# Performance work log

Measured on AMD Instinct MI355X. Metric: run time of the kernel, lower is better.

Reference implementation:

```python
import jax, jax.numpy as jnp
import numpy as np

B, LQ, LKV = 2, 2048, 2048
C, CTX, H, DK = 1024, 768, 16, 64
SCALE = DK ** (-0.5)


def setup_inputs() -> dict:
    key = jax.random.key(0)
    kx, ky, kq, kkv, kp, kb = jax.random.split(key, 6)
    # weights stored as [in, out] so projection is x @ W
    return {
        "x": jax.random.normal(kx, (B, LQ, C), dtype=jnp.float32),
        "y": jax.random.normal(ky, (B, LKV, CTX), dtype=jnp.float32),
        "Wq": jax.random.normal(kq, (C, H * DK), dtype=jnp.float32) * (C ** -0.5),
        "Wkv": jax.random.normal(kkv, (CTX, 2 * H * DK), dtype=jnp.float32) * (CTX ** -0.5),
        "Wproj": jax.random.normal(kp, (H * DK, C), dtype=jnp.float32) * ((H * DK) ** -0.5),
        "bproj": jax.random.normal(kb, (C,), dtype=jnp.float32) * 0.01,
    }


def reference(x, y, Wq, Wkv, Wproj, bproj):
    b, lq, _ = x.shape
    lkv = y.shape[1]
    # Q projection: [b, lq, H*DK] -> [b, H, lq, DK]
    q = (x @ Wq).reshape(b, lq, H, DK).transpose(0, 2, 1, 3)
    kv = (y @ Wkv).reshape(b, lkv, 2, H, DK).transpose(2, 0, 3, 1, 4)
    k, v = kv[0], kv[1]
    # attention scores [b, H, lq, lkv], stable softmax, no dropout (Identity)
    atten = jax.nn.softmax(jnp.einsum("bhid,bhjd->bhij", q, k) * SCALE, axis=-1)
    res = jnp.einsum("bhij,bhjd->bhid", atten, v)  # [b, H, lq, DK]
    res = res.transpose(0, 2, 1, 3).reshape(b, lq, H * DK)
    out = res @ Wproj + bproj  # [b, lq, C]
    return out
```

## Files before the change

kernel.cpp:

```cpp
#include <hip/hip_runtime.h>
#include <hip/hip_bf16.h>
#include <cstdint>

typedef unsigned short u16;
typedef __attribute__((ext_vector_type(4))) float f32x4;
typedef __attribute__((ext_vector_type(8))) short s16x8;
typedef __attribute__((ext_vector_type(4))) unsigned int u32x4;

#define B_    2
#define LQ_   2048
#define LKV_  2048
#define H_    16
#define QSCALE_ 0.18033688011112042f

__device__ __forceinline__ u16 f2b(float f) {
  union { float f; unsigned int u; } v; v.f = f;
  unsigned int r = v.u + 0x7fffu + ((v.u >> 16) & 1u);
  return (u16)(r >> 16);
}

__device__ __forceinline__ unsigned cvtpk(float lo, float hi) {
  unsigned r;
  asm("v_cvt_pk_bf16_f32 %0, %1, %2" : "=v"(r) : "v"(lo), "v"(hi));
  return r;
}

#if __has_builtin(__builtin_amdgcn_exp2f)
__device__ __forceinline__ float fexp2(float x) { return __builtin_amdgcn_exp2f(x); }
#else
__device__ __forceinline__ float fexp2(float x) {
  float r; asm volatile("v_exp_f32 %0, %1" : "=v"(r) : "v"(x)); return r;
}
#endif

#define GLOAD(g, l) __builtin_amdgcn_global_load_lds( \
    (const __attribute__((address_space(1))) void*)(g), \
    (__attribute__((address_space(3))) void*)(l), 16, 0, 0)

__global__ void prep(const float* __restrict__ x, u16* __restrict__ xb,
                     const float* __restrict__ y, u16* __restrict__ yb,
                     const float* __restrict__ Wq, u16* __restrict__ WqT,
                     const float* __restrict__ Wkv, u16* __restrict__ WkvT,
                     const float* __restrict__ Wp, u16* __restrict__ WpT) {
  __shared__ u16 tile[64][65];
  const int bid = blockIdx.x;
  const int t = threadIdx.x;
  if (bid < 7168) {
    const float* in; u16* out; int i;
    if (bid < 4096) { in = x; out = xb; i = (bid * 256 + t) * 4; }
    else            { in = y; out = yb; i = ((bid - 4096) * 256 + t) * 4; }
    float4 v = *reinterpret_cast<const float4*>(in + i);
    ushort4 r;
    r.x = f2b(v.x); r.y = f2b(v.y); r.z = f2b(v.z); r.w = f2b(v.w);
    *reinterpret_cast<ushort4*>(out + i) = r;
    return;
  }
  const int tb = bid - 7168;
  const float* W; u16* WT; int K, N, bx, by;
  if (tb < 256)      { W = Wq;  WT = WqT;  K = 1024; N = 1024; bx = tb & 15;         by = tb >> 4; }
  else if (tb < 640) { W = Wkv; WT = WkvT; K = 768;  N = 2048; bx = (tb - 256) & 31; by = (tb - 256) >> 5; }
  else               { W = Wp;  WT = WpT;  K = 1024; N = 1024; bx = (tb - 640) & 15; by = (tb - 640) >> 4; }
  const int n0 = bx * 64, k0 = by * 64;
#pragma unroll
  for (int p = 0; p < 4; ++p) {
    int r = (t >> 4) + p * 16;
    int c = (t & 15) * 4;
    float4 v = *reinterpret_cast<const float4*>(W + (size_t)(k0 + r) * N + n0 + c);
    tile[r][c + 0] = f2b(v.x);
    tile[r][c + 1] = f2b(v.y);
    tile[r][c + 2] = f2b(v.z);
    tile[r][c + 3] = f2b(v.w);
  }
  __syncthreads();
#pragma unroll
  for (int p = 0; p < 4; ++p) {
    int nr = (t >> 4) + p * 16;
    int kc = (t & 15) * 4;
    ushort4 o;
    o.x = tile[kc + 0][nr];
    o.y = tile[kc + 1][nr];
    o.z = tile[kc + 2][nr];
    o.w = tile[kc + 3][nr];
    *reinterpret_cast<ushort4*>(WT + (size_t)(n0 + nr) * K + k0 + kc) = o;
  }
}

template <int OM>
__global__ __launch_bounds__(256, 3)
void gemm_bt(const u16* __restrict__ A, const u16* __restrict__ BT,
             u16* __restrict__ Cb, float* __restrict__ Cf,
             const float* __restrict__ bias, u16* __restrict__ VTp,
             int M, int N, int K) {
  __shared__ __attribute__((aligned(16))) char smem[49152];
  const int tid = threadIdx.x;
  const int w = tid >> 6, lane = tid & 63;
  const int l16 = lane & 15, lk = lane >> 4;
  const int m0 = blockIdx.x * 128, n0 = blockIdx.y * 64;
  const int wm = w >> 1, ks = w & 1;
  const int K2 = K >> 1;
  const int NS = K2 >> 5;

  f32x4 acc[4][4];
#pragma unroll
  for (int i = 0; i < 4; ++i)
#pragma unroll
    for (int j = 0; j < 4; ++j)
      acc[i][j] = (f32x4){0.f, 0.f, 0.f, 0.f};

  const int srow = tid >> 2;
  const int sc = ((tid & 3) ^ ((tid >> 3) & 3)) * 8;
  const u16* gA0 = A + (size_t)(m0 + srow) * K + sc;
  const u16* gA1 = gA0 + K2;
  const u16* gB0 = BT + (size_t)(n0 + srow) * K + sc;
  const u16* gB1 = gB0 + K2;
  const size_t rstep = (size_t)64 * K;
  char* ldsA = smem;
  char* ldsB = smem + 32768;

  auto stage = [&](int k0, int bb) {
    GLOAD(gA0 + k0,         ldsA + bb * 8192 + w * 1024);
    GLOAD(gA0 + k0 + rstep, ldsA + bb * 8192 + 4096 + w * 1024);
    GLOAD(gA1 + k0,         ldsA + 16384 + bb * 8192 + w * 1024);
    GLOAD(gA1 + k0 + rstep, ldsA + 16384 + bb * 8192 + 4096 + w * 1024);
    GLOAD(gB0 + k0,         ldsB + bb * 4096 + w * 1024);
    GLOAD(gB1 + k0,         ldsB + 8192 + bb * 4096 + w * 1024);
  };

  const char* sAb = smem + ks * 16384;
  const char* sBb = smem + 32768 + ks * 8192;
  const int swl = ((l16 >> 1) & 3) << 4;

  stage(0, 0);
  __syncthreads();
  int cur = 0;
  for (int s = 0; s < NS; ++s) {
    if (s + 1 < NS) stage((s + 1) * 32, cur ^ 1);
    s16x8 af[4], bf[4];
#pragma unroll
    for (int mt = 0; mt < 4; ++mt)
      af[mt] = *reinterpret_cast<const s16x8*>(
          sAb + cur * 8192 + (wm * 64 + mt * 16 + l16) * 64 + ((lk * 16) ^ swl));
#pragma unroll
    for (int nt = 0; nt < 4; ++nt)
      bf[nt] = *reinterpret_cast<const s16x8*>(
          sBb + cur * 4096 + (nt * 16 + l16) * 64 + ((lk * 16) ^ swl));
    __builtin_amdgcn_s_setprio(1);
#pragma unroll
    for (int mt = 0; mt < 4; ++mt)
#pragma unroll
      for (int nt = 0; nt < 4; ++nt)
        acc[mt][nt] = __builtin_amdgcn_mfma_f32_16x16x32_bf16(af[mt], bf[nt], acc[mt][nt], 0, 0, 0);
    __builtin_amdgcn_s_setprio(0);
    __syncthreads();
    cur ^= 1;
  }

  if (ks == 1) {
    float* mb = reinterpret_cast<float*>(smem) + wm * 4096;
#pragma unroll
    for (int mt = 0; mt < 4; ++mt)
#pragma unroll
      for (int nt = 0; nt < 4; ++nt)
        *reinterpret_cast<f32x4*>(mb + ((mt * 4 + nt) * 64 + lane) * 4) = acc[mt][nt];
  }
  __syncthreads();
  if (ks == 1) return;
  {
    const float* mb = reinterpret_cast<const float*>(smem) + wm * 4096;
#pragma unroll
    for (int mt = 0; mt < 4; ++mt)
#pragma unroll
      for (int nt = 0; nt < 4; ++nt)
        acc[mt][nt] += *reinterpret_cast<const f32x4*>(mb + ((mt * 4 + nt) * 64 + lane) * 4);
  }

#pragma unroll
  for (int mt = 0; mt < 4; ++mt) {
#pragma unroll
    for (int nt = 0; nt < 4; ++nt) {
      const int col = n0 + nt * 16 + l16;
      const int row0 = m0 + wm * 64 + mt * 16 + lk * 4;
      if (OM == 2 && col >= 1024) {
        int b = row0 >> 11, kv = row0 & 2047;
        int h = (col >> 6) & 15, d = col & 63;
        ushort4 o;
        o.x = f2b(acc[mt][nt][0]); o.y = f2b(acc[mt][nt][1]);
        o.z = f2b(acc[mt][nt][2]); o.w = f2b(acc[mt][nt][3]);
        *reinterpret_cast<ushort4*>(VTp + (((size_t)(b * 16 + h) * 64 + d) * 2048 + kv)) = o;
      } else {
#pragma unroll
        for (int j = 0; j < 4; ++j) {
          int row = row0 + j;
          if (OM == 3)      Cb[(size_t)row * N + col] = f2b(acc[mt][nt][j] * QSCALE_);
          else if (OM == 2) Cb[(size_t)row * 1024 + col] = f2b(acc[mt][nt][j]);
          else              Cf[(size_t)row * N + col] = acc[mt][nt][j] + bias[col];
        }
      }
    }
  }
}

__global__ __launch_bounds__(512, 4)
void flash_attn(const u16* __restrict__ Kq, const u16* __restrict__ Qb,
                const u16* __restrict__ VT, u16* __restrict__ Rb) {
  __shared__ __attribute__((aligned(16))) char smem[65536];
  __shared__ float dmerge[512 * 2];

  const int tid = threadIdx.x;
  const int w = tid >> 6, l = tid & 63;
  const int l16 = l & 15, lk = l >> 4;
  const int half = w >> 2, w4 = w & 3;

  const int bid = blockIdx.x;
  const int wg = ((bid & 7) << 6) | (bid >> 3);
  const int qt = wg & 15, bh = wg >> 4;
  const int b = bh >> 4, h = bh & 15;
  const int qrow0 = qt * 128 + w4 * 32;

  const u16* qp = Qb + ((size_t)(b * LQ_ + qrow0 + l16)) * 1024 + h * 64;
  s16x8 qf[2][2];
#pragma unroll
  for (int g = 0; g < 2; ++g)
#pragma unroll
    for (int ksq = 0; ksq < 2; ++ksq)
      qf[g][ksq] = *reinterpret_cast<const s16x8*>(qp + g * 16 * 1024 + ksq * 32 + lk * 8);

  f32x4 Oacc[2][4], Osum[2];
#pragma unroll
  for (int g = 0; g < 2; ++g) {
    Osum[g] = (f32x4){0.f, 0.f, 0.f, 0.f};
#pragma unroll
    for (int dt = 0; dt < 4; ++dt) Oacc[g][dt] = (f32x4){0.f, 0.f, 0.f, 0.f};
  }

  const u16* Kg = Kq + ((size_t)(b * LKV_ + half * 1024)) * 1024 + h * 64;
  const u16* Vg = VT + ((size_t)bh * 64) * 2048 + half * 1024;
  char* Kl = smem + half * 32768;
  char* Vl = smem + half * 32768 + 16384;

  s16x8 ones;
#pragma unroll
  for (int i = 0; i < 8; ++i) ones[i] = (short)0x3F80;

  const int r0 = ((l16 >> 2) << 3) + (l16 & 3);
  const int swk = ((l16 & 3) | (((l16 >> 2) & 1) << 2)) << 4;
  const int swv = (l16 & 7) << 4;

  const int srow = (tid & 255) >> 3;
  const int sck = (tid & 7) ^ ((srow & 3) | (((srow >> 3) & 1) << 2));
  const int scv = (tid & 7) ^ (srow & 7);
  const u16* kp0 = Kg + (size_t)srow * 1024 + sck * 8;
  const u16* kp1 = kp0 + (size_t)32 * 1024;
  const u16* vp0 = Vg + (size_t)srow * 2048 + scv * 8;
  const u16* vp1 = vp0 + (size_t)32 * 2048;
  char* kd0 = Kl + w4 * 1024;
  char* vd0 = Vl + w4 * 1024;

  auto stage = [&](int bb) {
    GLOAD(kp0, kd0 + bb * 8192);
    GLOAD(kp1, kd0 + bb * 8192 + 4096);
    GLOAD(vp0, vd0 + bb * 8192);
    GLOAD(vp1, vd0 + bb * 8192 + 4096);
  };

  stage(0);
  kp0 += 65536; kp1 += 65536; vp0 += 64; vp1 += 64;
  __syncthreads();

  int cur = 0;
  for (int jt = 0; jt < 16; ++jt) {
    if (jt < 15) {
      stage(cur ^ 1);
      kp0 += 65536; kp1 += 65536; vp0 += 64; vp1 += 64;
    }
    const char* kb = Kl + cur * 8192;
    const char* vb = Vl + cur * 8192;

    f32x4 sacc[2][4];
#pragma unroll
    for (int g = 0; g < 2; ++g)
#pragma unroll
      for (int ct = 0; ct < 4; ++ct) sacc[g][ct] = (f32x4){0.f, 0.f, 0.f, 0.f};

    __builtin_amdgcn_s_setprio(1);
#pragma unroll
    for (int ct = 0; ct < 4; ++ct) {
      const int R = r0 + ((ct & 1) << 2) + ((ct >> 1) << 5);
      const char* rp = kb + R * 128;
      s16x8 ka0 = *reinterpret_cast<const s16x8*>(rp + ((lk * 16) ^ swk));
      s16x8 ka1 = *reinterpret_cast<const s16x8*>(rp + ((64 + lk * 16) ^ swk));
      sacc[0][ct] = __builtin_amdgcn_mfma_f32_16x16x32_bf16(ka0, qf[0][0], sacc[0][ct], 0, 0, 0);
      sacc[0][ct] = __builtin_amdgcn_mfma_f32_16x16x32_bf16(ka1, qf[0][1], sacc[0][ct], 0, 0, 0);
      sacc[1][ct] = __builtin_amdgcn_mfma_f32_16x16x32_bf16(ka0, qf[1][0], sacc[1][ct], 0, 0, 0);
      sacc[1][ct] = __builtin_amdgcn_mfma_f32_16x16x32_bf16(ka1, qf[1][1], sacc[1][ct], 0, 0, 0);
    }
    __builtin_amdgcn_s_setprio(0);

#pragma unroll
    for (int g = 0; g < 2; ++g)
#pragma unroll
      for (int ct = 0; ct < 4; ++ct)
#pragma unroll
        for (int j = 0; j < 4; ++j)
          sacc[g][ct][j] = fexp2(sacc[g][ct][j]);

#pragma unroll
    for (int f = 0; f < 2; ++f) {
      s16x8 va[4];
#pragma unroll
      for (int dt = 0; dt < 4; ++dt)
        va[dt] = *reinterpret_cast<const s16x8*>(vb + (dt * 16 + l16) * 128 + ((f * 64 + lk * 16) ^ swv));
      s16x8 pf[2];
#pragma unroll
      for (int g = 0; g < 2; ++g) {
        const f32x4 pA = sacc[g][2 * f];
        const f32x4 pB = sacc[g][2 * f + 1];
        union { unsigned u[4]; s16x8 v; } pk;
        pk.u[0] = cvtpk(pA[0], pA[1]);
        pk.u[1] = cvtpk(pA[2], pA[3]);
        pk.u[2] = cvtpk(pB[0], pB[1]);
        pk.u[3] = cvtpk(pB[2], pB[3]);
        pf[g] = pk.v;
      }
      __builtin_amdgcn_s_setprio(1);
#pragma unroll
      for (int dt = 0; dt < 4; ++dt) {
        Oacc[0][dt] = __builtin_amdgcn_mfma_f32_16x16x32_bf16(va[dt], pf[0], Oacc[0][dt], 0, 0, 0);
        Oacc[1][dt] = __builtin_amdgcn_mfma_f32_16x16x32_bf16(va[dt], pf[1], Oacc[1][dt], 0, 0, 0);
      }
      Osum[0] = __builtin_amdgcn_mfma_f32_16x16x32_bf16(ones, pf[0], Osum[0], 0, 0, 0);
      Osum[1] = __builtin_amdgcn_mfma_f32_16x16x32_bf16(ones, pf[1], Osum[1], 0, 0, 0);
      __builtin_amdgcn_s_setprio(0);
    }
    __syncthreads();
    cur ^= 1;
  }

  if (w >= 4) {
    char* mb = smem + (((w - 4) * 64 + l) * 128);
#pragma unroll
    for (int g = 0; g < 2; ++g)
#pragma unroll
      for (int dt = 0; dt < 4; ++dt)
        *reinterpret_cast<f32x4*>(mb + (((g * 4 + dt) * 16) ^ ((l & 7) << 4))) = Oacc[g][dt];
    dmerge[((w - 4) * 64 + l) * 2 + 0] = Osum[0][0];
    dmerge[((w - 4) * 64 + l) * 2 + 1] = Osum[1][0];
  }
  __syncthreads();
  if (w < 4) {
    const char* mb = smem + ((w * 64 + l) * 128);
#pragma unroll
    for (int g = 0; g < 2; ++g) {
      float inv = 1.f / (Osum[g][0] + dmerge[(w * 64 + l) * 2 + g]);
      u16* op = Rb + ((size_t)(b * LQ_ + qrow0 + g * 16 + l16)) * 1024 + h * 64 + lk * 4;
#pragma unroll
      for (int dt = 0; dt < 4; ++dt) {
        f32x4 o2 = *reinterpret_cast<const f32x4*>(mb + (((g * 4 + dt) * 16) ^ ((l & 7) << 4)));
        f32x4 s = Oacc[g][dt] + o2;
        ushort4 o;
        o.x = f2b(s[0] * inv); o.y = f2b(s[1] * inv);
        o.z = f2b(s[2] * inv); o.w = f2b(s[3] * inv);
        *reinterpret_cast<ushort4*>(op + dt * 16) = o;
      }
    }
  }
}

extern "C" void kernel_launch(void* const* d_in, const int* in_sizes, int n_in,
                              void* d_out, int out_size, void* d_ws, size_t ws_size,
                              hipStream_t stream) {
  const float* x   = (const float*)d_in[0];
  const float* y   = (const float*)d_in[1];
  const float* Wq  = (const float*)d_in[2];
  const float* Wkv = (const float*)d_in[3];
  const float* Wp  = (const float*)d_in[4];
  const float* bp  = (const float*)d_in[5];
  float* out = (float*)d_out;

  u16* p = (u16*)d_ws;
  u16* xb   = p; p += (size_t)4096 * 1024;
  u16* yb   = p; p += (size_t)4096 * 768;
  u16* WqT  = p; p += (size_t)1024 * 1024;
  u16* WkvT = p; p += (size_t)2048 * 768;
  u16* WpT  = p; p += (size_t)1024 * 1024;
  u16* Qb   = p; p += (size_t)4096 * 1024;
  u16* Kbf  = p; p += (size_t)4096 * 1024;
  u16* VTb  = p; p += (size_t)4096 * 1024;
  u16* Rb   = p; p += (size_t)4096 * 1024;

  prep<<<8064, 256, 0, stream>>>(x, xb, y, yb, Wq, WqT, Wkv, WkvT, Wp, WpT);

  gemm_bt<3><<<dim3(32, 16), 256, 0, stream>>>(xb, WqT, Qb, nullptr, nullptr, nullptr, 4096, 1024, 1024);
  gemm_bt<2><<<dim3(32, 32), 256, 0, stream>>>(yb, WkvT, Kbf, nullptr, nullptr, VTb, 4096, 2048, 768);
  flash_attn<<<512, 512, 0, stream>>>(Kbf, Qb, VTb, Rb);
  gemm_bt<1><<<dim3(32, 16), 256, 0, stream>>>(Rb, WpT, nullptr, out, bp, nullptr, 4096, 1024, 1024);
}
```

Baseline: 121.0 us.

## Merge Q and KV projection GEMMs into one launch and drop split-K warps

The Q and KV projection GEMMs now run as a single 1536-block launch, with the block index choosing which problem each block computes. This removes one kernel launch and its tail, and lets the two GEMMs fill the GPU together. The GEMM core also drops the intra-block split-K scheme (two K-halves plus an LDS reduction). Each of the 4 warps now owns a 64x32 output tile and works on a 64-wide K stage with a new 8-way XOR swizzle. This removes the reduction's LDS round trip and barrier, but gives each warp fewer MFMAs per fragment load.

```diff
diff --git a/kernel.cpp b/kernel.cpp
--- a/kernel.cpp
+++ b/kernel.cpp
@@ -85,100 +85,77 @@
   }
 }
 
-template <int OM>
-__global__ __launch_bounds__(256, 3)
-void gemm_bt(const u16* __restrict__ A, const u16* __restrict__ BT,
-             u16* __restrict__ Cb, float* __restrict__ Cf,
-             const float* __restrict__ bias, u16* __restrict__ VTp,
-             int M, int N, int K) {
-  __shared__ __attribute__((aligned(16))) char smem[49152];
+__device__ __forceinline__ void gemm_core(
+    int OM, const u16* __restrict__ A, const u16* __restrict__ BT,
+    u16* __restrict__ Cb, float* __restrict__ Cf,
+    const float* __restrict__ bias, u16* __restrict__ VTp,
+    int N, int K, int m0, int n0, char* smem) {
   const int tid = threadIdx.x;
   const int w = tid >> 6, lane = tid & 63;
   const int l16 = lane & 15, lk = lane >> 4;
-  const int m0 = blockIdx.x * 128, n0 = blockIdx.y * 64;
-  const int wm = w >> 1, ks = w & 1;
-  const int K2 = K >> 1;
-  const int NS = K2 >> 5;
-
-  f32x4 acc[4][4];
+  const int wm = w >> 1, wn = w & 1;
+  const int NS = K >> 6;
+
+  f32x4 acc[4][2];
 #pragma unroll
   for (int i = 0; i < 4; ++i)
 #pragma unroll
-    for (int j = 0; j < 4; ++j)
+    for (int j = 0; j < 2; ++j)
       acc[i][j] = (f32x4){0.f, 0.f, 0.f, 0.f};
 
-  const int srow = tid >> 2;
-  const int sc = ((tid & 3) ^ ((tid >> 3) & 3)) * 8;
-  const u16* gA0 = A + (size_t)(m0 + srow) * K + sc;
-  const u16* gA1 = gA0 + K2;
-  const u16* gB0 = BT + (size_t)(n0 + srow) * K + sc;
-  const u16* gB1 = gB0 + K2;
-  const size_t rstep = (size_t)64 * K;
-  char* ldsA = smem;
-  char* ldsB = smem + 32768;
+  const int srow = tid >> 3;
+  const int sck = (tid & 7) ^ (srow & 7);
+  const u16* gA = A + (size_t)(m0 + srow) * K + sck * 8;
+  const u16* gB = BT + (size_t)(n0 + srow) * K + sck * 8;
+  char* dA = smem + w * 1024;
+  char* dB = smem + 32768 + w * 1024;
 
   auto stage = [&](int k0, int bb) {
-    GLOAD(gA0 + k0,         ldsA + bb * 8192 + w * 1024);
-    GLOAD(gA0 + k0 + rstep, ldsA + bb * 8192 + 4096 + w * 1024);
-    GLOAD(gA1 + k0,         ldsA + 16384 + bb * 8192 + w * 1024);
-    GLOAD(gA1 + k0 + rstep, ldsA + 16384 + bb * 8192 + 4096 + w * 1024);
-    GLOAD(gB0 + k0,         ldsB + bb * 4096 + w * 1024);
-    GLOAD(gB1 + k0,         ldsB + 8192 + bb * 4096 + w * 1024);
+#pragma unroll
+    for (int i = 0; i < 4; ++i)
+      GLOAD(gA + (size_t)i * 32 * K + k0, dA + bb * 16384 + i * 4096);
+#pragma unroll
+    for (int i = 0; i < 2; ++i)
+      GLOAD(gB + (size_t)i * 32 * K + k0, dB + bb * 8192 + i * 4096);
   };
 
-  const char* sAb = smem + ks * 16384;
-  const char* sBb = smem + 32768 + ks * 8192;
-  const int swl = ((l16 >> 1) & 3) << 4;
+  const int swa = (l16 & 7) << 4;
 
   stage(0, 0);
   __syncthreads();
   int cur = 0;
   for (int s = 0; s < NS; ++s) {
-    if (s + 1 < NS) stage((s + 1) * 32, cur ^ 1);
-    s16x8 af[4], bf[4];
-#pragma unroll
-    for (int mt = 0; mt < 4; ++mt)
-      af[mt] = *reinterpret_cast<const s16x8*>(
-          sAb + cur * 8192 + (wm * 64 + mt * 16 + l16) * 64 + ((lk * 16) ^ swl));
-#pragma unroll
-    for (int nt = 0; nt < 4; ++nt)
-      bf[nt] = *reinterpret_cast<const s16x8*>(
-          sBb + cur * 4096 + (nt * 16 + l16) * 64 + ((lk * 16) ^ swl));
-    __builtin_amdgcn_s_setprio(1);
-#pragma unroll
-    for (int mt = 0; mt < 4; ++mt)
-#pragma unroll
-      for (int nt = 0; nt < 4; ++nt)
-        acc[mt][nt] = __builtin_amdgcn_mfma_f32_16x16x32_bf16(af[mt], bf[nt], acc[mt][nt], 0, 0, 0);
-    __builtin_amdgcn_s_setprio(0);
+    if (s + 1 < NS) stage((s + 1) * 64, cur ^ 1);
+    const char* sAb = smem + cur * 16384;
+    const char* sBb = smem + 32768 + cur * 8192;
+#pragma unroll
+    for (int kk = 0; kk < 2; ++kk) {
+      s16x8 af[4], bf[2];
+#pragma unroll
+      for (int mt = 0; mt < 4; ++mt)
+        af[mt] = *reinterpret_cast<const s16x8*>(
+            sAb + (wm * 64 + mt * 16 + l16) * 128 + ((kk * 64 + lk * 16) ^ swa));
+#pragma unroll
+      for (int nt = 0; nt < 2; ++nt)
+        bf[nt] = *reinterpret_cast<const s16x8*>(
+            sBb + (wn * 32 + nt * 16 + l16) * 128 + ((kk * 64 + lk * 16) ^ swa));
+      __builtin_amdgcn_s_setprio(1);
+#pragma unroll
+      for (int mt = 0; mt < 4; ++mt)
+#pragma unroll
+        for (int nt = 0; nt < 2; ++nt)
+          acc[mt][nt] = __builtin_amdgcn_mfma_f32_16x16x32_bf16(af[mt], bf[nt], acc[mt][nt], 0, 0, 0);
+      __builtin_amdgcn_s_setprio(0);
+    }
     __syncthreads();
     cur ^= 1;
   }
 
-  if (ks == 1) {
-    float* mb = reinterpret_cast<float*>(smem) + wm * 4096;
-#pragma unroll
-    for (int mt = 0; mt < 4; ++mt)
-#pragma unroll
-      for (int nt = 0; nt < 4; ++nt)
-        *reinterpret_cast<f32x4*>(mb + ((mt * 4 + nt) * 64 + lane) * 4) = acc[mt][nt];
-  }
-  __syncthreads();
-  if (ks == 1) return;
-  {
-    const float* mb = reinterpret_cast<const float*>(smem) + wm * 4096;
-#pragma unroll
-    for (int mt = 0; mt < 4; ++mt)
-#pragma unroll
-      for (int nt = 0; nt < 4; ++nt)
-        acc[mt][nt] += *reinterpret_cast<const f32x4*>(mb + ((mt * 4 + nt) * 64 + lane) * 4);
-  }
-
 #pragma unroll
   for (int mt = 0; mt < 4; ++mt) {
 #pragma unroll
-    for (int nt = 0; nt < 4; ++nt) {
-      const int col = n0 + nt * 16 + l16;
+    for (int nt = 0; nt < 2; ++nt) {
+      const int col = n0 + wn * 32 + nt * 16 + l16;
       const int row0 = m0 + wm * 64 + mt * 16 + lk * 4;
       if (OM == 2 && col >= 1024) {
         int b = row0 >> 11, kv = row0 & 2047;
@@ -198,6 +175,31 @@
       }
     }
   }
+}
+
+__global__ __launch_bounds__(256, 3)
+void gemm_qkv(const u16* __restrict__ xb, const u16* __restrict__ WqT,
+              const u16* __restrict__ yb, const u16* __restrict__ WkvT,
+              u16* __restrict__ Qb, u16* __restrict__ Kbf, u16* __restrict__ VTb) {
+  __shared__ __attribute__((aligned(16))) char smem[49152];
+  const int bid = blockIdx.x;
+  if (bid < 512) {
+    gemm_core(3, xb, WqT, Qb, nullptr, nullptr, nullptr,
+              1024, 1024, (bid & 31) * 128, (bid >> 5) * 64, smem);
+  } else {
+    const int t = bid - 512;
+    gemm_core(2, yb, WkvT, Kbf, nullptr, nullptr, VTb,
+              2048, 768, (t & 31) * 128, (t >> 5) * 64, smem);
+  }
+}
+
+__global__ __launch_bounds__(256, 3)
+void gemm_proj(const u16* __restrict__ Rb, const u16* __restrict__ WpT,
+               float* __restrict__ out, const float* __restrict__ bias) {
+  __shared__ __attribute__((aligned(16))) char smem[49152];
+  const int bid = blockIdx.x;
+  gemm_core(1, Rb, WpT, nullptr, out, bias, nullptr,
+            1024, 1024, (bid & 31) * 128, (bid >> 5) * 64, smem);
 }
 
 __global__ __launch_bounds__(512, 4)
@@ -390,8 +392,7 @@
 
   prep<<<8064, 256, 0, stream>>>(x, xb, y, yb, Wq, WqT, Wkv, WkvT, Wp, WpT);
 
-  gemm_bt<3><<<dim3(32, 16), 256, 0, stream>>>(xb, WqT, Qb, nullptr, nullptr, nullptr, 4096, 1024, 1024);
-  gemm_bt<2><<<dim3(32, 32), 256, 0, stream>>>(yb, WkvT, Kbf, nullptr, nullptr, VTb, 4096, 2048, 768);
+  gemm_qkv<<<1536, 256, 0, stream>>>(xb, WqT, yb, WkvT, Qb, Kbf, VTb);
   flash_attn<<<512, 512, 0, stream>>>(Kbf, Qb, VTb, Rb);
-  gemm_bt<1><<<dim3(32, 16), 256, 0, stream>>>(Rb, WpT, nullptr, out, bp, nullptr, 4096, 1024, 1024);
-}
+  gemm_proj<<<512, 256, 0, stream>>>(Rb, WpT, out, bp);
+}
```

Measured after the change: 99.73 us (median of 2 runs). 17.6% less time.
